# Performance work log

Hardware: AMD Instinct MI355X
Metric: run time of the kernel (lower is better)

Reference implementation:

```python
import jax, jax.numpy as jnp
import numpy as np

B, T, IN, H, OUT = 256, 100, 128, 1024, 35
BITS = 4
SLOPE = 25.0
THR_H = 1.0
THR_O = 1.0
BETA1, BETA2, BETA3, BETA4 = 0.9, 0.85, 0.8, 0.95


def fake_quant(w, w_min, w_max, bits=BITS):
    # FakeQuantize in training mode: STE -> forward value is quantized, grad passes through clamp
    levels = 2 ** bits
    scale = (w_max - w_min) / (levels - 1)
    wc = jnp.clip(w, w_min, w_max)
    q = jnp.round((wc - w_min) / scale) * scale + w_min
    return wc + jax.lax.stop_gradient(q - wc)


@jax.custom_vjp
def spike(x):
    # Heaviside forward, fast-sigmoid surrogate backward (snn.surrogate.fast_sigmoid)
    return (x > 0).astype(x.dtype)

def _spike_fwd(x):
    return (x > 0).astype(x.dtype), x

def _spike_bwd(x, g):
    return (g / (SLOPE * jnp.abs(x) + 1.0) ** 2,)

spike.defvjp(_spike_fwd, _spike_bwd)


def lif_step(cur, mem, beta, thr, reset_mechanism):
    # snntorch Leaky (reset_delay semantics): reset computed from previous mem, detached
    reset = jax.lax.stop_gradient((mem > thr).astype(cur.dtype))
    base = beta * mem + cur
    if reset_mechanism == "subtract":
        mem_new = base - reset * thr
    else:  # "zero"
        mem_new = base - reset * base
    spk = spike(mem_new - thr)
    return spk, mem_new


def setup_inputs() -> dict:
    key = jax.random.key(0)
    ks = jax.random.split(key, 5)
    x = jax.random.normal(ks[0], (B, T, IN), dtype=jnp.float32)
    # QuantLinear init: uniform(w_min, w_max); fc1 uses (-0.5, 0.5), others (0.001, 1.0)
    w1 = jax.random.uniform(ks[1], (H, IN), minval=-0.5, maxval=0.5, dtype=jnp.float32)
    w2 = jax.random.uniform(ks[2], (H, H), minval=0.001, maxval=1.0, dtype=jnp.float32)
    w3 = jax.random.uniform(ks[3], (H, H), minval=0.001, maxval=1.0, dtype=jnp.float32)
    w4 = jax.random.uniform(ks[4], (OUT, H), minval=0.001, maxval=1.0, dtype=jnp.float32)
    return {"x": x, "w1": w1, "w2": w2, "w3": w3, "w4": w4}


def reference(x, w1, w2, w3, w4):
    # hoist weight quantization out of the time loop (identical math each step)
    q1 = fake_quant(w1, -0.5, 0.5)
    q2 = fake_quant(w2, 0.001, 1.0)
    q3 = fake_quant(w3, 0.001, 1.0)
    q4 = fake_quant(w4, 0.001, 1.0)
    xs = jnp.transpose(x, (1, 0, 2)) / 15.0  # [T, B, IN]
    Bx = x.shape[0]

    def step(carry, xt):
        m1, m2, m3, m4 = carry
        s1, m1 = lif_step(xt @ q1.T, m1, BETA1, THR_H, "subtract")
        s2, m2 = lif_step(s1 @ q2.T, m2, BETA2, THR_H, "subtract")
        s3, m3 = lif_step(s2 @ q3.T, m3, BETA3, THR_H, "subtract")
        s4, m4 = lif_step(s3 @ q4.T, m4, BETA4, THR_O, "zero")
        return (m1, m2, m3, m4), (s1, s2, s3, s4, m4)

    init = (jnp.zeros((Bx, H), x.dtype), jnp.zeros((Bx, H), x.dtype),
            jnp.zeros((Bx, H), x.dtype), jnp.zeros((Bx, OUT), x.dtype))
    _, (spk1, spk2, spk3, spk4, mem4) = jax.lax.scan(step, init, xs)
    # stacked along time dim 0, matching torch.stack(dim=0)
    return spk1, spk2, spk3, spk4, mem4
```

## Files before the change

### kernel.cpp

```cpp
#include <hip/hip_runtime.h>
#include <stdint.h>

#define NB  256
#define NT  100
#define NIN 128
#define NH  1024
#define NOUT 35

#define O_SPK2 26214400ull
#define O_SPK3 52428800ull
#define O_SPK4 78643200ull
#define O_MEM4 79539200ull

#define WS_XT   0ull
#define WS_Q1T  13107200ull
#define WS_K2T  13631488ull
#define WS_K3T  14680064ull
#define WS_K4T  15728640ull
#define WS_RS2  15777792ull
#define WS_RS3  15781888ull
#define WS_RS4  15785984ull

#define S2C ((float)((1.0 - 0.001) / 15.0))
#define S1C ((float)(1.0 / 15.0))

__global__ void k_prep(const float* __restrict__ x, const float* __restrict__ w1,
                       const float* __restrict__ w2, const float* __restrict__ w3,
                       const float* __restrict__ w4, uint8_t* __restrict__ ws)
{
  long long id = (long long)blockIdx.x * 256 + threadIdx.x;
  if (id < 1048576) {
    int i = (int)(id >> 10), j = (int)(id & 1023);
    float wv = w2[(size_t)j * 1024 + i];
    float wc = fminf(fmaxf(wv, 0.001f), 1.0f);
    ws[WS_K2T + id] = (uint8_t)(int)rintf((wc - 0.001f) / S2C);
    return;
  }
  id -= 1048576;
  if (id < 1048576) {
    int i = (int)(id >> 10), j = (int)(id & 1023);
    float wv = w3[(size_t)j * 1024 + i];
    float wc = fminf(fmaxf(wv, 0.001f), 1.0f);
    ws[WS_K3T + id] = (uint8_t)(int)rintf((wc - 0.001f) / S2C);
    return;
  }
  id -= 1048576;
  if (id < 49152) {
    int i = (int)(id / 48), j = (int)(id % 48);
    uint8_t v = 0;
    if (j < NOUT) {
      float wv = w4[(size_t)j * 1024 + i];
      float wc = fminf(fmaxf(wv, 0.001f), 1.0f);
      v = (uint8_t)(int)rintf((wc - 0.001f) / S2C);
    }
    ws[WS_K4T + id] = v;
    return;
  }
  id -= 49152;
  if (id < 131072) {
    int i = (int)(id >> 10), j = (int)(id & 1023);
    float wv = w1[(size_t)j * 128 + i];
    float wc = fminf(fmaxf(wv, -0.5f), 0.5f);
    float q = rintf((wc + 0.5f) / S1C) * S1C - 0.5f;
    ((float*)(ws + WS_Q1T))[id] = q;
    return;
  }
  id -= 131072;
  if (id < 3276800) {
    int row = (int)(id >> 7), i = (int)(id & 127);
    int tt = row >> 8, bb = row & 255;
    ((float*)(ws + WS_XT))[id] = x[((size_t)bb * NT + tt) * NIN + i] / 15.0f;
  }
}

__global__ void k_rowsum(const float* __restrict__ w2, const float* __restrict__ w3,
                         const float* __restrict__ w4, uint8_t* __restrict__ ws)
{
  int bid = blockIdx.x, tid = threadIdx.x;
  const float* W;
  uint32_t* o;
  if (bid < 1024)      { W = w2 + (size_t)bid * 1024;          o = (uint32_t*)(ws + WS_RS2) + bid; }
  else if (bid < 2048) { W = w3 + (size_t)(bid - 1024) * 1024; o = (uint32_t*)(ws + WS_RS3) + (bid - 1024); }
  else                 { W = w4 + (size_t)(bid - 2048) * 1024; o = (uint32_t*)(ws + WS_RS4) + (bid - 2048); }
  uint32_t s = 0;
  for (int i = tid; i < 1024; i += 256) {
    float wc = fminf(fmaxf(W[i], 0.001f), 1.0f);
    s += (uint32_t)(int)rintf((wc - 0.001f) / S2C);
  }
  #pragma unroll
  for (int off = 32; off; off >>= 1) s += (uint32_t)__shfl_down((int)s, off);
  __shared__ uint32_t red[4];
  if ((tid & 63) == 0) red[tid >> 6] = s;
  __syncthreads();
  if (tid == 0) *o = red[0] + red[1] + red[2] + red[3];
}

__global__ __launch_bounds__(512, 1) void k_spk1(const float* __restrict__ xt,
                                                 const float* __restrict__ q1T,
                                                 float* __restrict__ out)
{
  __shared__ float xs[25 * 128];
  const int b = blockIdx.x;
  const int tid = threadIdx.x;
  float m1a = 0.f, m1b = 0.f;

  for (int c = 0; c < 4; ++c) {
    __syncthreads();
    {
      int e = tid;
      int tt = e >> 5, iq = e & 31;
      ((float4*)xs)[e] = *(const float4*)(xt + ((size_t)(c * 25 + tt) * NB + b) * NIN + iq * 4);
      e = tid + 512;
      if (e < 800) {
        tt = e >> 5; iq = e & 31;
        ((float4*)xs)[e] = *(const float4*)(xt + ((size_t)(c * 25 + tt) * NB + b) * NIN + iq * 4);
      }
    }
    __syncthreads();

    float acc0[25], acc1[25];
    #pragma unroll
    for (int tt = 0; tt < 25; ++tt) { acc0[tt] = 0.f; acc1[tt] = 0.f; }

    for (int ib = 0; ib < 16; ++ib) {
      float q0[8], q1v[8];
      #pragma unroll
      for (int u = 0; u < 8; ++u) {
        q0[u]  = q1T[(size_t)(ib * 8 + u) * NH + tid];
        q1v[u] = q1T[(size_t)(ib * 8 + u) * NH + tid + 512];
      }
      #pragma unroll
      for (int tt = 0; tt < 25; ++tt) {
        const float4 xa = *(const float4*)&xs[tt * 128 + ib * 8];
        const float4 xb = *(const float4*)&xs[tt * 128 + ib * 8 + 4];
        acc0[tt] = fmaf(xa.x, q0[0], acc0[tt]);
        acc0[tt] = fmaf(xa.y, q0[1], acc0[tt]);
        acc0[tt] = fmaf(xa.z, q0[2], acc0[tt]);
        acc0[tt] = fmaf(xa.w, q0[3], acc0[tt]);
        acc0[tt] = fmaf(xb.x, q0[4], acc0[tt]);
        acc0[tt] = fmaf(xb.y, q0[5], acc0[tt]);
        acc0[tt] = fmaf(xb.z, q0[6], acc0[tt]);
        acc0[tt] = fmaf(xb.w, q0[7], acc0[tt]);
        acc1[tt] = fmaf(xa.x, q1v[0], acc1[tt]);
        acc1[tt] = fmaf(xa.y, q1v[1], acc1[tt]);
        acc1[tt] = fmaf(xa.z, q1v[2], acc1[tt]);
        acc1[tt] = fmaf(xa.w, q1v[3], acc1[tt]);
        acc1[tt] = fmaf(xb.x, q1v[4], acc1[tt]);
        acc1[tt] = fmaf(xb.y, q1v[5], acc1[tt]);
        acc1[tt] = fmaf(xb.z, q1v[6], acc1[tt]);
        acc1[tt] = fmaf(xb.w, q1v[7], acc1[tt]);
      }
    }
    #pragma unroll
    for (int tt = 0; tt < 25; ++tt) {
      const int t = c * 25 + tt;
      const size_t row = ((size_t)t * NB + b) * (size_t)NH;
      float rst0 = m1a > 1.0f ? 1.0f : 0.0f;
      m1a = fmaf(0.9f, m1a, acc0[tt]) - rst0;
      out[row + tid] = ((m1a - 1.0f) > 0.0f) ? 1.0f : 0.0f;
      float rst1 = m1b > 1.0f ? 1.0f : 0.0f;
      m1b = fmaf(0.9f, m1b, acc1[tt]) - rst1;
      out[row + tid + 512] = ((m1b - 1.0f) > 0.0f) ? 1.0f : 0.0f;
    }
  }
}

__global__ __launch_bounds__(1024, 1) void k_main(
    const uint8_t* __restrict__ k2T, const uint8_t* __restrict__ k3T,
    const uint8_t* __restrict__ k4T, const uint32_t* __restrict__ rs2,
    const uint32_t* __restrict__ rs3, const uint32_t* __restrict__ rs4,
    float* __restrict__ out)
{
  const int b = blockIdx.x;
  const int tid = threadIdx.x;
  const int lane = tid & 63;
  const int wave = tid >> 6;

  __shared__ uint16_t list[1024];
  __shared__ uint4    pEa4[1024];
  __shared__ uint4    pOa4[1024];
  __shared__ uint4    wcnt4[4];
  __shared__ uint32_t lpos;
  uint32_t* pEa  = (uint32_t*)pEa4;
  uint32_t* pOa  = (uint32_t*)pOa4;
  uint32_t* wcnt = (uint32_t*)wcnt4;

  float m2 = 0.f, m3 = 0.f, m4 = 0.f;
  const uint32_t r2v = rs2[tid];
  const uint32_t r3v = rs3[tid];
  const uint32_t r4v = (tid < NOUT) ? rs4[tid] : 0u;

  auto sumcnt = [&]() -> uint32_t {
    uint4 a0 = wcnt4[0], a1 = wcnt4[1], a2 = wcnt4[2], a3 = wcnt4[3];
    return a0.x + a0.y + a0.z + a0.w + a1.x + a1.y + a1.z + a1.w +
           a2.x + a2.y + a2.z + a2.w + a3.x + a3.y + a3.z + a3.w;
  };

  auto writeList = [&](uint64_t cw) {
    uint32_t cnt = (uint32_t)__popcll(cw);
    uint32_t bs = 0;
    if (lane == 0) bs = atomicAdd(&lpos, cnt);
    bs = (uint32_t)__shfl((int)bs, 0);
    if ((cw >> lane) & 1ull)
      list[bs + (uint32_t)__popcll(cw & ((1ull << lane) - 1ull))] = (uint16_t)tid;
  };

  auto gatherBig = [&](const uint8_t* __restrict__ mat, uint32_t nLv) {
    uint32_t aE0=0,aE1=0,aE2=0,aE3=0,aO0=0,aO1=0,aO2=0,aO3=0;
    const uint8_t* bp = mat + (lane << 4);
    uint32_t a = (uint32_t)wave;
    for (; a + 16 < nLv; a += 32) {
      uint32_t i0 = (uint32_t)__builtin_amdgcn_readfirstlane((int)list[a]);
      uint32_t i1 = (uint32_t)__builtin_amdgcn_readfirstlane((int)list[a + 16]);
      const uint4 w0 = *(const uint4*)(bp + ((size_t)i0 << 10));
      const uint4 w1 = *(const uint4*)(bp + ((size_t)i1 << 10));
      aE0 += w0.x & 0x00FF00FFu; aO0 += (w0.x >> 8) & 0x00FF00FFu;
      aE1 += w0.y & 0x00FF00FFu; aO1 += (w0.y >> 8) & 0x00FF00FFu;
      aE2 += w0.z & 0x00FF00FFu; aO2 += (w0.z >> 8) & 0x00FF00FFu;
      aE3 += w0.w & 0x00FF00FFu; aO3 += (w0.w >> 8) & 0x00FF00FFu;
      aE0 += w1.x & 0x00FF00FFu; aO0 += (w1.x >> 8) & 0x00FF00FFu;
      aE1 += w1.y & 0x00FF00FFu; aO1 += (w1.y >> 8) & 0x00FF00FFu;
      aE2 += w1.z & 0x00FF00FFu; aO2 += (w1.z >> 8) & 0x00FF00FFu;
      aE3 += w1.w & 0x00FF00FFu; aO3 += (w1.w >> 8) & 0x00FF00FFu;
    }
    if (a < nLv) {
      uint32_t i0 = (uint32_t)__builtin_amdgcn_readfirstlane((int)list[a]);
      const uint4 w0 = *(const uint4*)(bp + ((size_t)i0 << 10));
      aE0 += w0.x & 0x00FF00FFu; aO0 += (w0.x >> 8) & 0x00FF00FFu;
      aE1 += w0.y & 0x00FF00FFu; aO1 += (w0.y >> 8) & 0x00FF00FFu;
      aE2 += w0.z & 0x00FF00FFu; aO2 += (w0.z >> 8) & 0x00FF00FFu;
      aE3 += w0.w & 0x00FF00FFu; aO3 += (w0.w >> 8) & 0x00FF00FFu;
    }
    const int basei = (wave << 8) + (lane << 2);
    *(uint4*)&pEa[basei] = make_uint4(aE0, aE1, aE2, aE3);
    *(uint4*)&pOa[basei] = make_uint4(aO0, aO1, aO2, aO3);
  };

  auto gsum = [&](int jn) -> uint32_t {
    int w = jn >> 2, sh = (jn & 2) << 3;
    const uint32_t* P = (jn & 1) ? pOa : pEa;
    uint32_t s = 0;
    #pragma unroll
    for (int g = 0; g < 16; ++g) s += (P[(g << 8) + w] >> sh) & 0xffffu;
    return s;
  };

  float s1v = out[(size_t)b * NH + tid];
  uint32_t nT, nL; bool cm;

  for (int t = 0; t < NT; ++t) {
    const size_t rowH = ((size_t)t * NB + b) * (size_t)NH;
    const size_t rowO = ((size_t)t * NB + b) * (size_t)NOUT;

    bool sA = s1v > 0.5f;
    {
      int tn = (t + 1 < NT) ? (t + 1) : t;
      s1v = out[((size_t)tn * NB + b) * (size_t)NH + tid];
    }
    uint64_t b1 = __ballot(sA);
    if (tid == 0) lpos = 0;
    if (lane == 0) wcnt[wave] = (uint32_t)__popcll(b1);
    __syncthreads();
    nT = sumcnt(); cm = nT > 512; nL = cm ? 1024u - nT : nT;
    writeList(cm ? ~b1 : b1);
    __syncthreads();
    const uint32_t n1 = nT, nl1 = nL; const bool cm1 = cm;
    if (nl1) gatherBig(k2T, nl1);
    __syncthreads();

    bool sp;
    {
      uint32_t gsv = nl1 ? gsum(tid) : 0u;
      uint32_t K = cm1 ? (r2v - gsv) : gsv;
      float cur = fmaf(S2C, (float)K, 0.001f * (float)n1);
      float rst = m2 > 1.0f ? 1.0f : 0.0f;
      m2 = fmaf(0.85f, m2, cur) - rst;
      sp = (m2 - 1.0f) > 0.0f;
      out[O_SPK2 + rowH + tid] = sp ? 1.0f : 0.0f;
    }
    uint64_t b2 = __ballot(sp);
    if (tid == 0) lpos = 0;
    if (lane == 0) wcnt[wave] = (uint32_t)__popcll(b2);
    __syncthreads();
    nT = sumcnt(); cm = nT > 512; nL = cm ? 1024u - nT : nT;
    writeList(cm ? ~b2 : b2);
    __syncthreads();
    const uint32_t n2 = nT, nl2 = nL; const bool cm2 = cm;
    if (nl2) gatherBig(k3T, nl2);
    __syncthreads();

    {
      uint32_t gsv = nl2 ? gsum(tid) : 0u;
      uint32_t K = cm2 ? (r3v - gsv) : gsv;
      float cur = fmaf(S2C, (float)K, 0.001f * (float)n2);
      float rst = m3 > 1.0f ? 1.0f : 0.0f;
      m3 = fmaf(0.8f, m3, cur) - rst;
      sp = (m3 - 1.0f) > 0.0f;
      out[O_SPK3 + rowH + tid] = sp ? 1.0f : 0.0f;
    }
    uint64_t b3 = __ballot(sp);
    if (tid == 0) lpos = 0;
    if (lane == 0) wcnt[wave] = (uint32_t)__popcll(b3);
    __syncthreads();
    nT = sumcnt(); cm = nT > 512; nL = cm ? 1024u - nT : nT;
    writeList(cm ? ~b3 : b3);
    __syncthreads();
    const uint32_t n3 = nT, nl3 = nL; const bool cm3 = cm;

    if (nl3 && lane < 3) {
      uint32_t aE0=0,aE1=0,aE2=0,aE3=0,aO0=0,aO1=0,aO2=0,aO3=0;
      const uint8_t* bp = k4T + (lane << 4);
      for (uint32_t a = (uint32_t)wave; a < nl3; a += 16) {
        uint32_t i0 = (uint32_t)__builtin_amdgcn_readfirstlane((int)list[a]);
        const uint4 w0 = *(const uint4*)(bp + (size_t)i0 * 48u);
        aE0 += w0.x & 0x00FF00FFu; aO0 += (w0.x >> 8) & 0x00FF00FFu;
        aE1 += w0.y & 0x00FF00FFu; aO1 += (w0.y >> 8) & 0x00FF00FFu;
        aE2 += w0.z & 0x00FF00FFu; aO2 += (w0.z >> 8) & 0x00FF00FFu;
        aE3 += w0.w & 0x00FF00FFu; aO3 += (w0.w >> 8) & 0x00FF00FFu;
      }
      const int basei = (wave << 8) + (lane << 2);
      *(uint4*)&pEa[basei] = make_uint4(aE0, aE1, aE2, aE3);
      *(uint4*)&pOa[basei] = make_uint4(aO0, aO1, aO2, aO3);
    }
    __syncthreads();

    if (tid < NOUT) {
      uint32_t gsv = nl3 ? gsum(tid) : 0u;
      uint32_t K = cm3 ? (r4v - gsv) : gsv;
      float cur = fmaf(S2C, (float)K, 0.001f * (float)n3);
      float rst = m4 > 1.0f ? 1.0f : 0.0f;
      float bsv = fmaf(0.95f, m4, cur);
      m4 = (rst > 0.0f) ? 0.0f : bsv;
      out[O_SPK4 + rowO + tid] = ((m4 - 1.0f) > 0.0f) ? 1.0f : 0.0f;
      out[O_MEM4 + rowO + tid] = m4;
    }
  }
}

extern "C" void kernel_launch(void* const* d_in, const int* in_sizes, int n_in,
                              void* d_out, int out_size, void* d_ws, size_t ws_size,
                              hipStream_t stream)
{
  const float* x  = (const float*)d_in[0];
  const float* w1 = (const float*)d_in[1];
  const float* w2 = (const float*)d_in[2];
  const float* w3 = (const float*)d_in[3];
  const float* w4 = (const float*)d_in[4];
  float* out = (float*)d_out;
  uint8_t* ws = (uint8_t*)d_ws;
  hipLaunchKernelGGL(k_prep,   dim3(21696), dim3(256), 0, stream, x, w1, w2, w3, w4, ws);
  hipLaunchKernelGGL(k_rowsum, dim3(2083),  dim3(256), 0, stream, w2, w3, w4, ws);
  hipLaunchKernelGGL(k_spk1,   dim3(256),   dim3(512), 0, stream,
                     (const float*)(ws + WS_XT), (const float*)(ws + WS_Q1T), out);
  hipLaunchKernelGGL(k_main,   dim3(256),   dim3(1024), 0, stream,
                     ws + WS_K2T, ws + WS_K3T, ws + WS_K4T,
                     (const uint32_t*)(ws + WS_RS2), (const uint32_t*)(ws + WS_RS3),
                     (const uint32_t*)(ws + WS_RS4), out);
}
```

Before: 701.1 us.

## Tile weight transpose, drop x pre-transpose and rowsum kernel, deterministic list build

The weight quantize-transpose in k_prep now goes through a shared-memory tile so both the float reads and the byte writes are coalesced. The x pre-transpose pass is removed: k_spk1 reads x directly into registers and broadcasts elements with readlane instead of staging them in LDS. The separate rowsum kernel is replaced by full-matrix gathers at the start of k_main. The atomic-based spike list construction becomes a deterministic per-wave prefix sum, and the gather loops are unrolled four-wide. Together these cut launches and global traffic, at the cost of extra startup gathers per block and higher register pressure in k_spk1.

New measurement: 743.7 us. 1.06x slower.

```diff
diff --git a/kernel.cpp b/kernel.cpp
--- a/kernel.cpp
+++ b/kernel.cpp
@@ -17,34 +17,40 @@
 #define WS_K2T  13631488ull
 #define WS_K3T  14680064ull
 #define WS_K4T  15728640ull
-#define WS_RS2  15777792ull
-#define WS_RS3  15781888ull
-#define WS_RS4  15785984ull
 
 #define S2C ((float)((1.0 - 0.001) / 15.0))
 #define S1C ((float)(1.0 / 15.0))
 
-__global__ void k_prep(const float* __restrict__ x, const float* __restrict__ w1,
+__global__ __launch_bounds__(256) void k_prep(const float* __restrict__ w1,
                        const float* __restrict__ w2, const float* __restrict__ w3,
                        const float* __restrict__ w4, uint8_t* __restrict__ ws)
 {
-  long long id = (long long)blockIdx.x * 256 + threadIdx.x;
-  if (id < 1048576) {
-    int i = (int)(id >> 10), j = (int)(id & 1023);
-    float wv = w2[(size_t)j * 1024 + i];
-    float wc = fminf(fmaxf(wv, 0.001f), 1.0f);
-    ws[WS_K2T + id] = (uint8_t)(int)rintf((wc - 0.001f) / S2C);
+  const int bid = blockIdx.x, tid = threadIdx.x;
+  if (bid < 512) {
+    const float* W = (bid < 256) ? w2 : w3;
+    uint8_t* K = ws + ((bid < 256) ? WS_K2T : WS_K3T);
+    const int tb = bid & 255;
+    const int i0 = (tb & 15) << 6, j0 = (tb >> 4) << 6;
+    __shared__ uint8_t tile[64 * 68];
+    const int jl = tid >> 4, iq = (tid & 15) << 2;
+    #pragma unroll
+    for (int k = 0; k < 4; ++k) {
+      const int jloc = jl + k * 16;
+      const float4 v = *(const float4*)&W[(size_t)(j0 + jloc) * 1024 + i0 + iq];
+      float wc;
+      wc = fminf(fmaxf(v.x, 0.001f), 1.0f); tile[(iq + 0) * 68 + jloc] = (uint8_t)(int)rintf((wc - 0.001f) / S2C);
+      wc = fminf(fmaxf(v.y, 0.001f), 1.0f); tile[(iq + 1) * 68 + jloc] = (uint8_t)(int)rintf((wc - 0.001f) / S2C);
+      wc = fminf(fmaxf(v.z, 0.001f), 1.0f); tile[(iq + 2) * 68 + jloc] = (uint8_t)(int)rintf((wc - 0.001f) / S2C);
+      wc = fminf(fmaxf(v.w, 0.001f), 1.0f); tile[(iq + 3) * 68 + jloc] = (uint8_t)(int)rintf((wc - 0.001f) / S2C);
+    }
+    __syncthreads();
+    const int li = tid >> 2, cq = tid & 3;
+    const uint32_t* tp = (const uint32_t*)&tile[li * 68 + (cq << 4)];
+    *(uint4*)&K[(size_t)(i0 + li) * 1024 + j0 + (cq << 4)] =
+        make_uint4(tp[0], tp[1], tp[2], tp[3]);
     return;
   }
-  id -= 1048576;
-  if (id < 1048576) {
-    int i = (int)(id >> 10), j = (int)(id & 1023);
-    float wv = w3[(size_t)j * 1024 + i];
-    float wc = fminf(fmaxf(wv, 0.001f), 1.0f);
-    ws[WS_K3T + id] = (uint8_t)(int)rintf((wc - 0.001f) / S2C);
-    return;
-  }
-  id -= 1048576;
+  long long id = (long long)(bid - 512) * 256 + tid;
   if (id < 49152) {
     int i = (int)(id / 48), j = (int)(id % 48);
     uint8_t v = 0;
@@ -63,66 +69,33 @@
     float wc = fminf(fmaxf(wv, -0.5f), 0.5f);
     float q = rintf((wc + 0.5f) / S1C) * S1C - 0.5f;
     ((float*)(ws + WS_Q1T))[id] = q;
-    return;
-  }
-  id -= 131072;
-  if (id < 3276800) {
-    int row = (int)(id >> 7), i = (int)(id & 127);
-    int tt = row >> 8, bb = row & 255;
-    ((float*)(ws + WS_XT))[id] = x[((size_t)bb * NT + tt) * NIN + i] / 15.0f;
   }
 }
 
-__global__ void k_rowsum(const float* __restrict__ w2, const float* __restrict__ w3,
-                         const float* __restrict__ w4, uint8_t* __restrict__ ws)
-{
-  int bid = blockIdx.x, tid = threadIdx.x;
-  const float* W;
-  uint32_t* o;
-  if (bid < 1024)      { W = w2 + (size_t)bid * 1024;          o = (uint32_t*)(ws + WS_RS2) + bid; }
-  else if (bid < 2048) { W = w3 + (size_t)(bid - 1024) * 1024; o = (uint32_t*)(ws + WS_RS3) + (bid - 1024); }
-  else                 { W = w4 + (size_t)(bid - 2048) * 1024; o = (uint32_t*)(ws + WS_RS4) + (bid - 2048); }
-  uint32_t s = 0;
-  for (int i = tid; i < 1024; i += 256) {
-    float wc = fminf(fmaxf(W[i], 0.001f), 1.0f);
-    s += (uint32_t)(int)rintf((wc - 0.001f) / S2C);
-  }
-  #pragma unroll
-  for (int off = 32; off; off >>= 1) s += (uint32_t)__shfl_down((int)s, off);
-  __shared__ uint32_t red[4];
-  if ((tid & 63) == 0) red[tid >> 6] = s;
-  __syncthreads();
-  if (tid == 0) *o = red[0] + red[1] + red[2] + red[3];
-}
-
-__global__ __launch_bounds__(512, 1) void k_spk1(const float* __restrict__ xt,
+__global__ __launch_bounds__(512, 1) void k_spk1(const float* __restrict__ x,
                                                  const float* __restrict__ q1T,
                                                  float* __restrict__ out)
 {
-  __shared__ float xs[25 * 128];
   const int b = blockIdx.x;
   const int tid = threadIdx.x;
+  const int lane = tid & 63;
+  const float* xb = x + (size_t)b * NT * NIN;
   float m1a = 0.f, m1b = 0.f;
 
   for (int c = 0; c < 4; ++c) {
-    __syncthreads();
-    {
-      int e = tid;
-      int tt = e >> 5, iq = e & 31;
-      ((float4*)xs)[e] = *(const float4*)(xt + ((size_t)(c * 25 + tt) * NB + b) * NIN + iq * 4);
-      e = tid + 512;
-      if (e < 800) {
-        tt = e >> 5; iq = e & 31;
-        ((float4*)xs)[e] = *(const float4*)(xt + ((size_t)(c * 25 + tt) * NB + b) * NIN + iq * 4);
-      }
-    }
-    __syncthreads();
-
+    float xv0[25], xv1[25];
+    #pragma unroll
+    for (int tt = 0; tt < 25; ++tt) {
+      const float* xr = xb + (size_t)(c * 25 + tt) * NIN;
+      xv0[tt] = xr[lane] / 15.0f;
+      xv1[tt] = xr[lane + 64] / 15.0f;
+    }
     float acc0[25], acc1[25];
     #pragma unroll
     for (int tt = 0; tt < 25; ++tt) { acc0[tt] = 0.f; acc1[tt] = 0.f; }
 
-    for (int ib = 0; ib < 16; ++ib) {
+    #pragma unroll 2
+    for (int ib = 0; ib < 8; ++ib) {
       float q0[8], q1v[8];
       #pragma unroll
       for (int u = 0; u < 8; ++u) {
@@ -131,24 +104,30 @@
       }
       #pragma unroll
       for (int tt = 0; tt < 25; ++tt) {
-        const float4 xa = *(const float4*)&xs[tt * 128 + ib * 8];
-        const float4 xb = *(const float4*)&xs[tt * 128 + ib * 8 + 4];
-        acc0[tt] = fmaf(xa.x, q0[0], acc0[tt]);
-        acc0[tt] = fmaf(xa.y, q0[1], acc0[tt]);
-        acc0[tt] = fmaf(xa.z, q0[2], acc0[tt]);
-        acc0[tt] = fmaf(xa.w, q0[3], acc0[tt]);
-        acc0[tt] = fmaf(xb.x, q0[4], acc0[tt]);
-        acc0[tt] = fmaf(xb.y, q0[5], acc0[tt]);
-        acc0[tt] = fmaf(xb.z, q0[6], acc0[tt]);
-        acc0[tt] = fmaf(xb.w, q0[7], acc0[tt]);
-        acc1[tt] = fmaf(xa.x, q1v[0], acc1[tt]);
-        acc1[tt] = fmaf(xa.y, q1v[1], acc1[tt]);
-        acc1[tt] = fmaf(xa.z, q1v[2], acc1[tt]);
-        acc1[tt] = fmaf(xa.w, q1v[3], acc1[tt]);
-        acc1[tt] = fmaf(xb.x, q1v[4], acc1[tt]);
-        acc1[tt] = fmaf(xb.y, q1v[5], acc1[tt]);
-        acc1[tt] = fmaf(xb.z, q1v[6], acc1[tt]);
-        acc1[tt] = fmaf(xb.w, q1v[7], acc1[tt]);
+        #pragma unroll
+        for (int u = 0; u < 8; ++u) {
+          float xs = __int_as_float(__builtin_amdgcn_readlane(__float_as_int(xv0[tt]), ib * 8 + u));
+          acc0[tt] = fmaf(xs, q0[u], acc0[tt]);
+          acc1[tt] = fmaf(xs, q1v[u], acc1[tt]);
+        }
+      }
+    }
+    #pragma unroll 2
+    for (int ib = 8; ib < 16; ++ib) {
+      float q0[8], q1v[8];
+      #pragma unroll
+      for (int u = 0; u < 8; ++u) {
+        q0[u]  = q1T[(size_t)(ib * 8 + u) * NH + tid];
+        q1v[u] = q1T[(size_t)(ib * 8 + u) * NH + tid + 512];
+      }
+      #pragma unroll
+      for (int tt = 0; tt < 25; ++tt) {
+        #pragma unroll
+        for (int u = 0; u < 8; ++u) {
+          float xs = __int_as_float(__builtin_amdgcn_readlane(__float_as_int(xv1[tt]), ib * 8 + u - 64));
+          acc0[tt] = fmaf(xs, q0[u], acc0[tt]);
+          acc1[tt] = fmaf(xs, q1v[u], acc1[tt]);
+        }
       }
     }
     #pragma unroll
@@ -165,11 +144,15 @@
   }
 }
 
+#define ACC(V) do { \
+  aE0 += (V).x & 0x00FF00FFu; aO0 += ((V).x >> 8) & 0x00FF00FFu; \
+  aE1 += (V).y & 0x00FF00FFu; aO1 += ((V).y >> 8) & 0x00FF00FFu; \
+  aE2 += (V).z & 0x00FF00FFu; aO2 += ((V).z >> 8) & 0x00FF00FFu; \
+  aE3 += (V).w & 0x00FF00FFu; aO3 += ((V).w >> 8) & 0x00FF00FFu; } while (0)
+
 __global__ __launch_bounds__(1024, 1) void k_main(
     const uint8_t* __restrict__ k2T, const uint8_t* __restrict__ k3T,
-    const uint8_t* __restrict__ k4T, const uint32_t* __restrict__ rs2,
-    const uint32_t* __restrict__ rs3, const uint32_t* __restrict__ rs4,
-    float* __restrict__ out)
+    const uint8_t* __restrict__ k4T, float* __restrict__ out)
 {
   const int b = blockIdx.x;
   const int tid = threadIdx.x;
@@ -180,27 +163,31 @@
   __shared__ uint4    pEa4[1024];
   __shared__ uint4    pOa4[1024];
   __shared__ uint4    wcnt4[4];
-  __shared__ uint32_t lpos;
   uint32_t* pEa  = (uint32_t*)pEa4;
   uint32_t* pOa  = (uint32_t*)pOa4;
   uint32_t* wcnt = (uint32_t*)wcnt4;
 
   float m2 = 0.f, m3 = 0.f, m4 = 0.f;
-  const uint32_t r2v = rs2[tid];
-  const uint32_t r3v = rs3[tid];
-  const uint32_t r4v = (tid < NOUT) ? rs4[tid] : 0u;
-
-  auto sumcnt = [&]() -> uint32_t {
-    uint4 a0 = wcnt4[0], a1 = wcnt4[1], a2 = wcnt4[2], a3 = wcnt4[3];
-    return a0.x + a0.y + a0.z + a0.w + a1.x + a1.y + a1.z + a1.w +
-           a2.x + a2.y + a2.z + a2.w + a3.x + a3.y + a3.z + a3.w;
-  };
-
-  auto writeList = [&](uint64_t cw) {
-    uint32_t cnt = (uint32_t)__popcll(cw);
-    uint32_t bs = 0;
-    if (lane == 0) bs = atomicAdd(&lpos, cnt);
-    bs = (uint32_t)__shfl((int)bs, 0);
+  uint32_t nT, nL; bool cm;
+
+  auto buildList = [&](uint64_t bal) {
+    const uint4 c0 = wcnt4[0], c1 = wcnt4[1], c2 = wcnt4[2], c3 = wcnt4[3];
+    nT = c0.x + c0.y + c0.z + c0.w + c1.x + c1.y + c1.z + c1.w +
+         c2.x + c2.y + c2.z + c2.w + c3.x + c3.y + c3.z + c3.w;
+    cm = nT > 512;
+    nL = cm ? (1024u - nT) : nT;
+    uint32_t pre = 0;
+    const int w = wave;
+    pre += (w > 0)  ? c0.x : 0u;  pre += (w > 1)  ? c0.y : 0u;
+    pre += (w > 2)  ? c0.z : 0u;  pre += (w > 3)  ? c0.w : 0u;
+    pre += (w > 4)  ? c1.x : 0u;  pre += (w > 5)  ? c1.y : 0u;
+    pre += (w > 6)  ? c1.z : 0u;  pre += (w > 7)  ? c1.w : 0u;
+    pre += (w > 8)  ? c2.x : 0u;  pre += (w > 9)  ? c2.y : 0u;
+    pre += (w > 10) ? c2.z : 0u;  pre += (w > 11) ? c2.w : 0u;
+    pre += (w > 12) ? c3.x : 0u;  pre += (w > 13) ? c3.y : 0u;
+    pre += (w > 14) ? c3.z : 0u;
+    const uint32_t bs = cm ? ((uint32_t)(w << 6) - pre) : pre;
+    const uint64_t cw = cm ? ~bal : bal;
     if ((cw >> lane) & 1ull)
       list[bs + (uint32_t)__popcll(cw & ((1ull << lane) - 1ull))] = (uint16_t)tid;
   };
@@ -209,44 +196,104 @@
     uint32_t aE0=0,aE1=0,aE2=0,aE3=0,aO0=0,aO1=0,aO2=0,aO3=0;
     const uint8_t* bp = mat + (lane << 4);
     uint32_t a = (uint32_t)wave;
-    for (; a + 16 < nLv; a += 32) {
+    for (; a + 48 < nLv; a += 64) {
       uint32_t i0 = (uint32_t)__builtin_amdgcn_readfirstlane((int)list[a]);
       uint32_t i1 = (uint32_t)__builtin_amdgcn_readfirstlane((int)list[a + 16]);
-      const uint4 w0 = *(const uint4*)(bp + ((size_t)i0 << 10));
-      const uint4 w1 = *(const uint4*)(bp + ((size_t)i1 << 10));
-      aE0 += w0.x & 0x00FF00FFu; aO0 += (w0.x >> 8) & 0x00FF00FFu;
-      aE1 += w0.y & 0x00FF00FFu; aO1 += (w0.y >> 8) & 0x00FF00FFu;
-      aE2 += w0.z & 0x00FF00FFu; aO2 += (w0.z >> 8) & 0x00FF00FFu;
-      aE3 += w0.w & 0x00FF00FFu; aO3 += (w0.w >> 8) & 0x00FF00FFu;
-      aE0 += w1.x & 0x00FF00FFu; aO0 += (w1.x >> 8) & 0x00FF00FFu;
-      aE1 += w1.y & 0x00FF00FFu; aO1 += (w1.y >> 8) & 0x00FF00FFu;
-      aE2 += w1.z & 0x00FF00FFu; aO2 += (w1.z >> 8) & 0x00FF00FFu;
-      aE3 += w1.w & 0x00FF00FFu; aO3 += (w1.w >> 8) & 0x00FF00FFu;
-    }
-    if (a < nLv) {
+      uint32_t i2 = (uint32_t)__builtin_amdgcn_readfirstlane((int)list[a + 32]);
+      uint32_t i3 = (uint32_t)__builtin_amdgcn_readfirstlane((int)list[a + 48]);
+      const uint4 v0 = *(const uint4*)(bp + ((size_t)i0 << 10));
+      const uint4 v1 = *(const uint4*)(bp + ((size_t)i1 << 10));
+      const uint4 v2 = *(const uint4*)(bp + ((size_t)i2 << 10));
+      const uint4 v3 = *(const uint4*)(bp + ((size_t)i3 << 10));
+      ACC(v0); ACC(v1); ACC(v2); ACC(v3);
+    }
+    for (; a < nLv; a += 16) {
       uint32_t i0 = (uint32_t)__builtin_amdgcn_readfirstlane((int)list[a]);
-      const uint4 w0 = *(const uint4*)(bp + ((size_t)i0 << 10));
-      aE0 += w0.x & 0x00FF00FFu; aO0 += (w0.x >> 8) & 0x00FF00FFu;
-      aE1 += w0.y & 0x00FF00FFu; aO1 += (w0.y >> 8) & 0x00FF00FFu;
-      aE2 += w0.z & 0x00FF00FFu; aO2 += (w0.z >> 8) & 0x00FF00FFu;
-      aE3 += w0.w & 0x00FF00FFu; aO3 += (w0.w >> 8) & 0x00FF00FFu;
+      const uint4 v0 = *(const uint4*)(bp + ((size_t)i0 << 10));
+      ACC(v0);
     }
     const int basei = (wave << 8) + (lane << 2);
     *(uint4*)&pEa[basei] = make_uint4(aE0, aE1, aE2, aE3);
     *(uint4*)&pOa[basei] = make_uint4(aO0, aO1, aO2, aO3);
   };
 
+  auto gatherAll = [&](const uint8_t* __restrict__ mat) {
+    uint32_t aE0=0,aE1=0,aE2=0,aE3=0,aO0=0,aO1=0,aO2=0,aO3=0;
+    const uint8_t* bp = mat + (lane << 4);
+    for (uint32_t a = (uint32_t)wave; a + 48 < 1024u; a += 64) {
+      const uint4 v0 = *(const uint4*)(bp + ((size_t)a << 10));
+      const uint4 v1 = *(const uint4*)(bp + ((size_t)(a + 16) << 10));
+      const uint4 v2 = *(const uint4*)(bp + ((size_t)(a + 32) << 10));
+      const uint4 v3 = *(const uint4*)(bp + ((size_t)(a + 48) << 10));
+      ACC(v0); ACC(v1); ACC(v2); ACC(v3);
+    }
+    const int basei = (wave << 8) + (lane << 2);
+    *(uint4*)&pEa[basei] = make_uint4(aE0, aE1, aE2, aE3);
+    *(uint4*)&pOa[basei] = make_uint4(aO0, aO1, aO2, aO3);
+  };
+
+  auto gather4 = [&](uint32_t nLv) {
+    uint32_t aE0=0,aE1=0,aE2=0,aE3=0,aO0=0,aO1=0,aO2=0,aO3=0;
+    const uint8_t* bp = k4T + (lane << 4);
+    uint32_t a = (uint32_t)wave;
+    for (; a + 48 < nLv; a += 64) {
+      uint32_t i0 = (uint32_t)__builtin_amdgcn_readfirstlane((int)list[a]);
+      uint32_t i1 = (uint32_t)__builtin_amdgcn_readfirstlane((int)list[a + 16]);
+      uint32_t i2 = (uint32_t)__builtin_amdgcn_readfirstlane((int)list[a + 32]);
+      uint32_t i3 = (uint32_t)__builtin_amdgcn_readfirstlane((int)list[a + 48]);
+      const uint4 v0 = *(const uint4*)(bp + (size_t)i0 * 48u);
+      const uint4 v1 = *(const uint4*)(bp + (size_t)i1 * 48u);
+      const uint4 v2 = *(const uint4*)(bp + (size_t)i2 * 48u);
+      const uint4 v3 = *(const uint4*)(bp + (size_t)i3 * 48u);
+      ACC(v0); ACC(v1); ACC(v2); ACC(v3);
+    }
+    for (; a < nLv; a += 16) {
+      uint32_t i0 = (uint32_t)__builtin_amdgcn_readfirstlane((int)list[a]);
+      const uint4 v0 = *(const uint4*)(bp + (size_t)i0 * 48u);
+      ACC(v0);
+    }
+    const int basei = (wave << 8) + (lane << 2);
+    *(uint4*)&pEa[basei] = make_uint4(aE0, aE1, aE2, aE3);
+    *(uint4*)&pOa[basei] = make_uint4(aO0, aO1, aO2, aO3);
+  };
+
+  auto gather4All = [&]() {
+    uint32_t aE0=0,aE1=0,aE2=0,aE3=0,aO0=0,aO1=0,aO2=0,aO3=0;
+    const uint8_t* bp = k4T + (lane << 4);
+    for (uint32_t a = (uint32_t)wave; a + 48 < 1024u; a += 64) {
+      const uint4 v0 = *(const uint4*)(bp + (size_t)a * 48u);
+      const uint4 v1 = *(const uint4*)(bp + (size_t)(a + 16) * 48u);
+      const uint4 v2 = *(const uint4*)(bp + (size_t)(a + 32) * 48u);
+      const uint4 v3 = *(const uint4*)(bp + (size_t)(a + 48) * 48u);
+      ACC(v0); ACC(v1); ACC(v2); ACC(v3);
+    }
+    const int basei = (wave << 8) + (lane << 2);
+    *(uint4*)&pEa[basei] = make_uint4(aE0, aE1, aE2, aE3);
+    *(uint4*)&pOa[basei] = make_uint4(aO0, aO1, aO2, aO3);
+  };
+
   auto gsum = [&](int jn) -> uint32_t {
-    int w = jn >> 2, sh = (jn & 2) << 3;
+    const int w = jn >> 2, sh = (jn & 2) << 3;
     const uint32_t* P = (jn & 1) ? pOa : pEa;
     uint32_t s = 0;
     #pragma unroll
-    for (int g = 0; g < 16; ++g) s += (P[(g << 8) + w] >> sh) & 0xffffu;
-    return s;
-  };
+    for (int g = 0; g < 16; ++g) s += P[(g << 8) + w];
+    return (s >> sh) & 0xffffu;
+  };
+
+  gatherAll(k2T);
+  __syncthreads();
+  const uint32_t r2v = gsum(tid);
+  __syncthreads();
+  gatherAll(k3T);
+  __syncthreads();
+  const uint32_t r3v = gsum(tid);
+  __syncthreads();
+  if (lane < 3) gather4All();
+  __syncthreads();
+  const uint32_t r4v = (tid < NOUT) ? gsum(tid) : 0u;
 
   float s1v = out[(size_t)b * NH + tid];
-  uint32_t nT, nL; bool cm;
 
   for (int t = 0; t < NT; ++t) {
     const size_t rowH = ((size_t)t * NB + b) * (size_t)NH;
@@ -258,11 +305,9 @@
       s1v = out[((size_t)tn * NB + b) * (size_t)NH + tid];
     }
     uint64_t b1 = __ballot(sA);
-    if (tid == 0) lpos = 0;
     if (lane == 0) wcnt[wave] = (uint32_t)__popcll(b1);
     __syncthreads();
-    nT = sumcnt(); cm = nT > 512; nL = cm ? 1024u - nT : nT;
-    writeList(cm ? ~b1 : b1);
+    buildList(b1);
     __syncthreads();
     const uint32_t n1 = nT, nl1 = nL; const bool cm1 = cm;
     if (nl1) gatherBig(k2T, nl1);
@@ -279,11 +324,9 @@
       out[O_SPK2 + rowH + tid] = sp ? 1.0f : 0.0f;
     }
     uint64_t b2 = __ballot(sp);
-    if (tid == 0) lpos = 0;
     if (lane == 0) wcnt[wave] = (uint32_t)__popcll(b2);
     __syncthreads();
-    nT = sumcnt(); cm = nT > 512; nL = cm ? 1024u - nT : nT;
-    writeList(cm ? ~b2 : b2);
+    buildList(b2);
     __syncthreads();
     const uint32_t n2 = nT, nl2 = nL; const bool cm2 = cm;
     if (nl2) gatherBig(k3T, nl2);
@@ -299,29 +342,13 @@
       out[O_SPK3 + rowH + tid] = sp ? 1.0f : 0.0f;
     }
     uint64_t b3 = __ballot(sp);
-    if (tid == 0) lpos = 0;
     if (lane == 0) wcnt[wave] = (uint32_t)__popcll(b3);
     __syncthreads();
-    nT = sumcnt(); cm = nT > 512; nL = cm ? 1024u - nT : nT;
-    writeList(cm ? ~b3 : b3);
+    buildList(b3);
     __syncthreads();
     const uint32_t n3 = nT, nl3 = nL; const bool cm3 = cm;
 
-    if (nl3 && lane < 3) {
-      uint32_t aE0=0,aE1=0,aE2=0,aE3=0,aO0=0,aO1=0,aO2=0,aO3=0;
-      const uint8_t* bp = k4T + (lane << 4);
-      for (uint32_t a = (uint32_t)wave; a < nl3; a += 16) {
-        uint32_t i0 = (uint32_t)__builtin_amdgcn_readfirstlane((int)list[a]);
-        const uint4 w0 = *(const uint4*)(bp + (size_t)i0 * 48u);
-        aE0 += w0.x & 0x00FF00FFu; aO0 += (w0.x >> 8) & 0x00FF00FFu;
-        aE1 += w0.y & 0x00FF00FFu; aO1 += (w0.y >> 8) & 0x00FF00FFu;
-        aE2 += w0.z & 0x00FF00FFu; aO2 += (w0.z >> 8) & 0x00FF00FFu;
-        aE3 += w0.w & 0x00FF00FFu; aO3 += (w0.w >> 8) & 0x00FF00FFu;
-      }
-      const int basei = (wave << 8) + (lane << 2);
-      *(uint4*)&pEa[basei] = make_uint4(aE0, aE1, aE2, aE3);
-      *(uint4*)&pOa[basei] = make_uint4(aO0, aO1, aO2, aO3);
-    }
+    if (nl3 && lane < 3) gather4(nl3);
     __syncthreads();
 
     if (tid < NOUT) {
@@ -336,6 +363,7 @@
     }
   }
 }
+#undef ACC
 
 extern "C" void kernel_launch(void* const* d_in, const int* in_sizes, int n_in,
                               void* d_out, int out_size, void* d_ws, size_t ws_size,
@@ -348,12 +376,9 @@
   const float* w4 = (const float*)d_in[4];
   float* out = (float*)d_out;
   uint8_t* ws = (uint8_t*)d_ws;
-  hipLaunchKernelGGL(k_prep,   dim3(21696), dim3(256), 0, stream, x, w1, w2, w3, w4, ws);
-  hipLaunchKernelGGL(k_rowsum, dim3(2083),  dim3(256), 0, stream, w2, w3, w4, ws);
-  hipLaunchKernelGGL(k_spk1,   dim3(256),   dim3(512), 0, stream,
-                     (const float*)(ws + WS_XT), (const float*)(ws + WS_Q1T), out);
-  hipLaunchKernelGGL(k_main,   dim3(256),   dim3(1024), 0, stream,
-                     ws + WS_K2T, ws + WS_K3T, ws + WS_K4T,
-                     (const uint32_t*)(ws + WS_RS2), (const uint32_t*)(ws + WS_RS3),
-                     (const uint32_t*)(ws + WS_RS4), out);
+  hipLaunchKernelGGL(k_prep, dim3(1216), dim3(256), 0, stream, w1, w2, w3, w4, ws);
+  hipLaunchKernelGGL(k_spk1, dim3(256),  dim3(512), 0, stream,
+                     x, (const float*)(ws + WS_Q1T), out);
+  hipLaunchKernelGGL(k_main, dim3(256),  dim3(1024), 0, stream,
+                     ws + WS_K2T, ws + WS_K3T, ws + WS_K4T, out);
 }
```
